# Performance work log

Measured on AMD Instinct MI355X. Metric: run time of the kernel, lower is better.

Reference implementation:

```python
import jax, jax.numpy as jnp
import numpy as np

N_NODES = 100000
N_EDGES = 3200000
N_FEAT = 512
N_HID = 16
N_CLS = 7


def setup_inputs() -> dict:
    key = jax.random.key(0)
    k0, k1, k2, k3 = jax.random.split(key, 4)
    x = jax.random.normal(k0, (N_NODES, N_FEAT), dtype=jnp.float32)
    edge_index = jax.random.randint(k1, (2, N_EDGES), 0, N_NODES, dtype=jnp.int64)
    W1 = jax.random.normal(k2, (N_FEAT, N_HID), dtype=jnp.float32) * (1.0 / np.sqrt(N_FEAT))
    b1 = jnp.zeros((N_HID,), dtype=jnp.float32)
    W2 = jax.random.normal(k3, (N_HID, N_CLS), dtype=jnp.float32) * (1.0 / np.sqrt(N_HID))
    b2 = jnp.zeros((N_CLS,), dtype=jnp.float32)
    return {"x": x, "edge_index": edge_index, "W1": W1, "b1": b1, "W2": W2, "b2": b2}


def _graph_conv(x, src, dst, W, b, n_nodes):
    # transform-then-aggregate: keeps the gathered edge tensor at hidden width
    h = x @ W                                      # [N, out]
    agg = jax.ops.segment_sum(h[src], dst, num_segments=n_nodes)  # [N, out]
    return agg + b


def reference(x, edge_index, W1, b1, W2, b2):
    src, dst = edge_index[0], edge_index[1]
    h = jax.nn.relu(_graph_conv(x, src, dst, W1, b1, N_NODES))
    # dropout is identity in eval mode
    out = _graph_conv(h, src, dst, W2, b2, N_NODES)
    return jax.nn.log_softmax(out, axis=1)
```

## Files before the change

kernel.cpp:

```cpp
#include <hip/hip_runtime.h>

#define NN 100000
#define NE 3200000
#define NF 512
#define NH 16
#define NC 7

__global__ __launch_bounds__(256) void gemm1_kernel(const float* __restrict__ x,
                                                    const float* __restrict__ W1,
                                                    float* __restrict__ h0) {
  const int lane = threadIdx.x & 63;
  const int wave = (blockIdx.x * blockDim.x + threadIdx.x) >> 6;
  const int nwaves = (gridDim.x * blockDim.x) >> 6;

  float w[8][NH];
#pragma unroll
  for (int i = 0; i < 4; ++i) {
#pragma unroll
    for (int j = 0; j < NH; ++j) {
      w[i][j]     = W1[(4 * lane + i) * NH + j];
      w[4 + i][j] = W1[(256 + 4 * lane + i) * NH + j];
    }
  }

  for (int row = wave; row < NN; row += nwaves) {
    const float4* xr = (const float4*)(x + (size_t)row * NF);
    float4 a0 = xr[lane];
    float4 a1 = xr[64 + lane];
    float a[8] = {a0.x, a0.y, a0.z, a0.w, a1.x, a1.y, a1.z, a1.w};

    float acc[NH];
#pragma unroll
    for (int j = 0; j < NH; ++j) acc[j] = 0.f;
#pragma unroll
    for (int i = 0; i < 8; ++i) {
#pragma unroll
      for (int j = 0; j < NH; ++j) acc[j] += a[i] * w[i][j];
    }

    float outv = 0.f;
#pragma unroll
    for (int j = 0; j < NH; ++j) {
      float v = acc[j];
      v += __shfl_xor(v, 1);
      v += __shfl_xor(v, 2);
      v += __shfl_xor(v, 4);
      v += __shfl_xor(v, 8);
      v += __shfl_xor(v, 16);
      v += __shfl_xor(v, 32);
      if (lane == j) outv = v;
    }
    if (lane < NH) h0[(size_t)row * NH + lane] = outv;
  }
}

__global__ __launch_bounds__(256) void scatter16_kernel(const int* __restrict__ ei,
                                                        const float* __restrict__ h0,
                                                        float* __restrict__ agg) {
  long long gid = (long long)blockIdx.x * blockDim.x + threadIdx.x;
  int e = (int)(gid >> 4);
  if (e >= NE) return;
  int j = (int)(gid & 15);
  int s = ei[e];
  int d = ei[NE + e];
  atomicAdd(&agg[(size_t)d * NH + j], h0[(size_t)s * NH + j]);
}

__global__ __launch_bounds__(256) void transform_kernel(const float* __restrict__ agg1,
                                                        const float* __restrict__ b1,
                                                        const float* __restrict__ W2,
                                                        float* __restrict__ p) {
  int n = blockIdx.x * blockDim.x + threadIdx.x;
  if (n >= NN) return;
  const float4* r = (const float4*)(agg1 + (size_t)n * NH);
  float4 v0 = r[0], v1 = r[1], v2 = r[2], v3 = r[3];
  float h[NH] = {v0.x, v0.y, v0.z, v0.w, v1.x, v1.y, v1.z, v1.w,
                 v2.x, v2.y, v2.z, v2.w, v3.x, v3.y, v3.z, v3.w};
#pragma unroll
  for (int k = 0; k < NH; ++k) h[k] = fmaxf(h[k] + b1[k], 0.f);

#pragma unroll
  for (int j = 0; j < NC; ++j) {
    float acc = 0.f;
#pragma unroll
    for (int k = 0; k < NH; ++k) acc += h[k] * W2[k * NC + j];
    p[(size_t)n * 8 + j] = acc;
  }
}

__global__ __launch_bounds__(256) void scatter7_kernel(const int* __restrict__ ei,
                                                       const float* __restrict__ p,
                                                       float* __restrict__ agg) {
  long long gid = (long long)blockIdx.x * blockDim.x + threadIdx.x;
  int e = (int)(gid >> 3);
  if (e >= NE) return;
  int j = (int)(gid & 7);
  if (j >= NC) return;
  int s = ei[e];
  int d = ei[NE + e];
  atomicAdd(&agg[(size_t)d * 8 + j], p[(size_t)s * 8 + j]);
}

__global__ __launch_bounds__(256) void lsm_kernel(const float* __restrict__ agg2,
                                                  const float* __restrict__ b2,
                                                  float* __restrict__ out) {
  int n = blockIdx.x * blockDim.x + threadIdx.x;
  if (n >= NN) return;
  float z[NC];
  float m = -1e30f;
#pragma unroll
  for (int j = 0; j < NC; ++j) {
    z[j] = agg2[(size_t)n * 8 + j] + b2[j];
    m = fmaxf(m, z[j]);
  }
  float s = 0.f;
#pragma unroll
  for (int j = 0; j < NC; ++j) s += __expf(z[j] - m);
  float l = __logf(s);
#pragma unroll
  for (int j = 0; j < NC; ++j) out[(size_t)n * NC + j] = z[j] - m - l;
}

extern "C" void kernel_launch(void* const* d_in, const int* in_sizes, int n_in,
                              void* d_out, int out_size, void* d_ws, size_t ws_size,
                              hipStream_t stream) {
  const float* x  = (const float*)d_in[0];
  const int*   ei = (const int*)d_in[1];
  const float* W1 = (const float*)d_in[2];
  const float* b1 = (const float*)d_in[3];
  const float* W2 = (const float*)d_in[4];
  const float* b2 = (const float*)d_in[5];
  float* out = (float*)d_out;

  float* bufA = (float*)d_ws;
  float* bufB = bufA + (size_t)NN * NH;

  hipMemsetAsync(bufB, 0, (size_t)NN * NH * sizeof(float), stream);
  gemm1_kernel<<<2048, 256, 0, stream>>>(x, W1, bufA);
  scatter16_kernel<<<(int)(((long long)NE * 16 + 255) / 256), 256, 0, stream>>>(ei, bufA, bufB);
  transform_kernel<<<(NN + 255) / 256, 256, 0, stream>>>(bufB, b1, W2, bufA);
  hipMemsetAsync(bufB, 0, (size_t)NN * 8 * sizeof(float), stream);
  scatter7_kernel<<<(int)(((long long)NE * 8 + 255) / 256), 256, 0, stream>>>(ei, bufA, bufB);
  lsm_kernel<<<(NN + 255) / 256, 256, 0, stream>>>(bufB, b2, out);
}
```

Measured before the change: 704.9 us.

## Build CSR by destination each call and replace atomic scatters with pull aggregation

Each call now builds a destination-sorted CSR (degree histogram, multi-level scan, permutation of sources). Both graph aggregations become atomic-free per-node gather reductions, and the second aggregation is fused with log-softmax. The first GEMM processes two rows per wave with a transpose-style shuffle reduction that needs fewer shuffles. This removes 80M float atomics at the cost of two edge passes with integer atomics and several small extra launches.

```diff
diff --git a/kernel.cpp b/kernel.cpp
--- a/kernel.cpp
+++ b/kernel.cpp
@@ -5,65 +5,172 @@
 #define NF 512
 #define NH 16
 #define NC 7
+#define NB ((NN + 255) / 256)
+
+__device__ __forceinline__ float reduce16(const float acc[16], int lane) {
+  float w8[8];
+#pragma unroll
+  for (int i = 0; i < 8; ++i) {
+    float sel = (lane & 1) ? acc[2 * i + 1] : acc[2 * i];
+    float oth = (lane & 1) ? acc[2 * i]     : acc[2 * i + 1];
+    w8[i] = sel + __shfl_xor(oth, 1);
+  }
+  float w4[4];
+#pragma unroll
+  for (int i = 0; i < 4; ++i) {
+    float sel = (lane & 2) ? w8[2 * i + 1] : w8[2 * i];
+    float oth = (lane & 2) ? w8[2 * i]     : w8[2 * i + 1];
+    w4[i] = sel + __shfl_xor(oth, 2);
+  }
+  float w2[2];
+#pragma unroll
+  for (int i = 0; i < 2; ++i) {
+    float sel = (lane & 4) ? w4[2 * i + 1] : w4[2 * i];
+    float oth = (lane & 4) ? w4[2 * i]     : w4[2 * i + 1];
+    w2[i] = sel + __shfl_xor(oth, 4);
+  }
+  float sel = (lane & 8) ? w2[1] : w2[0];
+  float oth = (lane & 8) ? w2[0] : w2[1];
+  float v = sel + __shfl_xor(oth, 8);
+  v += __shfl_xor(v, 16);
+  v += __shfl_xor(v, 32);
+  return v;
+}
 
 __global__ __launch_bounds__(256) void gemm1_kernel(const float* __restrict__ x,
                                                     const float* __restrict__ W1,
                                                     float* __restrict__ h0) {
   const int lane = threadIdx.x & 63;
   const int wave = (blockIdx.x * blockDim.x + threadIdx.x) >> 6;
-  const int nwaves = (gridDim.x * blockDim.x) >> 6;
+  const int nw   = (gridDim.x * blockDim.x) >> 6;
 
   float w[8][NH];
 #pragma unroll
-  for (int i = 0; i < 4; ++i) {
+  for (int i = 0; i < 4; ++i)
 #pragma unroll
     for (int j = 0; j < NH; ++j) {
       w[i][j]     = W1[(4 * lane + i) * NH + j];
       w[4 + i][j] = W1[(256 + 4 * lane + i) * NH + j];
     }
-  }
-
-  for (int row = wave; row < NN; row += nwaves) {
-    const float4* xr = (const float4*)(x + (size_t)row * NF);
-    float4 a0 = xr[lane];
-    float4 a1 = xr[64 + lane];
-    float a[8] = {a0.x, a0.y, a0.z, a0.w, a1.x, a1.y, a1.z, a1.w};
-
-    float acc[NH];
-#pragma unroll
-    for (int j = 0; j < NH; ++j) acc[j] = 0.f;
-#pragma unroll
-    for (int i = 0; i < 8; ++i) {
-#pragma unroll
-      for (int j = 0; j < NH; ++j) acc[j] += a[i] * w[i][j];
-    }
-
-    float outv = 0.f;
-#pragma unroll
-    for (int j = 0; j < NH; ++j) {
-      float v = acc[j];
-      v += __shfl_xor(v, 1);
-      v += __shfl_xor(v, 2);
-      v += __shfl_xor(v, 4);
-      v += __shfl_xor(v, 8);
-      v += __shfl_xor(v, 16);
-      v += __shfl_xor(v, 32);
-      if (lane == j) outv = v;
-    }
-    if (lane < NH) h0[(size_t)row * NH + lane] = outv;
-  }
-}
-
-__global__ __launch_bounds__(256) void scatter16_kernel(const int* __restrict__ ei,
-                                                        const float* __restrict__ h0,
-                                                        float* __restrict__ agg) {
-  long long gid = (long long)blockIdx.x * blockDim.x + threadIdx.x;
-  int e = (int)(gid >> 4);
+
+  for (int pr = wave; pr < NN / 2; pr += nw) {
+    int r0 = 2 * pr;
+    const float4* x0 = (const float4*)(x + (size_t)r0 * NF);
+    const float4* x1 = (const float4*)(x + (size_t)(r0 + 1) * NF);
+    float4 a0 = x0[lane], b0 = x0[64 + lane];
+    float4 a1 = x1[lane], b1 = x1[64 + lane];
+    float A0[8] = {a0.x, a0.y, a0.z, a0.w, b0.x, b0.y, b0.z, b0.w};
+    float A1[8] = {a1.x, a1.y, a1.z, a1.w, b1.x, b1.y, b1.z, b1.w};
+    float c0[NH], c1[NH];
+#pragma unroll
+    for (int j = 0; j < NH; ++j) { c0[j] = 0.f; c1[j] = 0.f; }
+#pragma unroll
+    for (int i = 0; i < 8; ++i)
+#pragma unroll
+      for (int j = 0; j < NH; ++j) {
+        c0[j] += A0[i] * w[i][j];
+        c1[j] += A1[i] * w[i][j];
+      }
+    float v0 = reduce16(c0, lane);
+    float v1 = reduce16(c1, lane);
+    if (lane < 16)      h0[(size_t)r0 * NH + lane] = v0;
+    else if (lane < 32) h0[(size_t)(r0 + 1) * NH + (lane & 15)] = v1;
+  }
+}
+
+__global__ __launch_bounds__(256) void hist_kernel(const int* __restrict__ ei,
+                                                   int* __restrict__ degcur) {
+  int e = blockIdx.x * blockDim.x + threadIdx.x;
+  if (e < NE) atomicAdd(&degcur[ei[NE + e]], 1);
+}
+
+__global__ __launch_bounds__(256) void bsum_kernel(const int* __restrict__ deg,
+                                                   int* __restrict__ bsum) {
+  int i = blockIdx.x * blockDim.x + threadIdx.x;
+  int lane = threadIdx.x & 63, wid = threadIdx.x >> 6;
+  int v = (i < NN) ? deg[i] : 0;
+#pragma unroll
+  for (int m = 1; m < 64; m <<= 1) v += __shfl_xor(v, m);
+  __shared__ int ws[4];
+  if (lane == 0) ws[wid] = v;
+  __syncthreads();
+  if (threadIdx.x == 0) bsum[blockIdx.x] = ws[0] + ws[1] + ws[2] + ws[3];
+}
+
+__global__ __launch_bounds__(512) void bscan_kernel(const int* __restrict__ bsum,
+                                                    int* __restrict__ boff) {
+  __shared__ int tmp[512];
+  int tid = threadIdx.x;
+  int v = (tid < NB) ? bsum[tid] : 0;
+  tmp[tid] = v;
+  __syncthreads();
+  for (int off = 1; off < 512; off <<= 1) {
+    int t = (tid >= off) ? tmp[tid - off] : 0;
+    __syncthreads();
+    tmp[tid] += t;
+    __syncthreads();
+  }
+  boff[tid] = tmp[tid] - v;
+}
+
+__global__ __launch_bounds__(256) void scan_final_kernel(int* __restrict__ degcur,
+                                                         const int* __restrict__ boff,
+                                                         int* __restrict__ rowstart) {
+  int i = blockIdx.x * blockDim.x + threadIdx.x;
+  int lane = threadIdx.x & 63, wid = threadIdx.x >> 6;
+  int v = (i < NN) ? degcur[i] : 0;
+  int sv = v;
+#pragma unroll
+  for (int d = 1; d < 64; d <<= 1) {
+    int t = __shfl_up(sv, d);
+    if (lane >= d) sv += t;
+  }
+  __shared__ int wsum[4];
+  if (lane == 63) wsum[wid] = sv;
+  __syncthreads();
+  int woff = 0;
+  for (int w = 0; w < wid; ++w) woff += wsum[w];
+  int excl = sv - v + woff + boff[blockIdx.x];
+  if (i < NN) {
+    rowstart[i] = excl;
+    degcur[i]   = excl;
+    if (i == NN - 1) rowstart[NN] = excl + v;
+  }
+}
+
+__global__ __launch_bounds__(256) void permute_kernel(const int* __restrict__ ei,
+                                                      int* __restrict__ cursor,
+                                                      int* __restrict__ ssrc) {
+  int e = blockIdx.x * blockDim.x + threadIdx.x;
   if (e >= NE) return;
-  int j = (int)(gid & 15);
-  int s = ei[e];
-  int d = ei[NE + e];
-  atomicAdd(&agg[(size_t)d * NH + j], h0[(size_t)s * NH + j]);
+  int s = ei[e], d = ei[NE + e];
+  int pos = atomicAdd(&cursor[d], 1);
+  ssrc[pos] = s;
+}
+
+__global__ __launch_bounds__(256) void agg1_kernel(const int* __restrict__ rowstart,
+                                                   const int* __restrict__ ssrc,
+                                                   const float* __restrict__ h0,
+                                                   float* __restrict__ agg1) {
+  int n = (blockIdx.x * blockDim.x + threadIdx.x) >> 6;
+  if (n >= NN) return;
+  int lane = threadIdx.x & 63;
+  int eg = lane >> 2, c = lane & 3;
+  int start = rowstart[n], end = rowstart[n + 1];
+  float4 acc = {0.f, 0.f, 0.f, 0.f};
+  for (int e = start + eg; e < end; e += 16) {
+    int s = ssrc[e];
+    float4 hv = *(const float4*)(h0 + (size_t)s * NH + 4 * c);
+    acc.x += hv.x; acc.y += hv.y; acc.z += hv.z; acc.w += hv.w;
+  }
+#pragma unroll
+  for (int m = 4; m < 64; m <<= 1) {
+    acc.x += __shfl_xor(acc.x, m);
+    acc.y += __shfl_xor(acc.y, m);
+    acc.z += __shfl_xor(acc.z, m);
+    acc.w += __shfl_xor(acc.w, m);
+  }
+  if (lane < 4) *(float4*)(agg1 + (size_t)n * NH + 4 * lane) = acc;
 }
 
 __global__ __launch_bounds__(256) void transform_kernel(const float* __restrict__ agg1,
@@ -78,7 +185,6 @@
                  v2.x, v2.y, v2.z, v2.w, v3.x, v3.y, v3.z, v3.w};
 #pragma unroll
   for (int k = 0; k < NH; ++k) h[k] = fmaxf(h[k] + b1[k], 0.f);
-
 #pragma unroll
   for (int j = 0; j < NC; ++j) {
     float acc = 0.f;
@@ -86,39 +192,35 @@
     for (int k = 0; k < NH; ++k) acc += h[k] * W2[k * NC + j];
     p[(size_t)n * 8 + j] = acc;
   }
-}
-
-__global__ __launch_bounds__(256) void scatter7_kernel(const int* __restrict__ ei,
+  p[(size_t)n * 8 + 7] = 0.f;
+}
+
+__global__ __launch_bounds__(256) void agg2_lsm_kernel(const int* __restrict__ rowstart,
+                                                       const int* __restrict__ ssrc,
                                                        const float* __restrict__ p,
-                                                       float* __restrict__ agg) {
-  long long gid = (long long)blockIdx.x * blockDim.x + threadIdx.x;
-  int e = (int)(gid >> 3);
-  if (e >= NE) return;
-  int j = (int)(gid & 7);
-  if (j >= NC) return;
-  int s = ei[e];
-  int d = ei[NE + e];
-  atomicAdd(&agg[(size_t)d * 8 + j], p[(size_t)s * 8 + j]);
-}
-
-__global__ __launch_bounds__(256) void lsm_kernel(const float* __restrict__ agg2,
-                                                  const float* __restrict__ b2,
-                                                  float* __restrict__ out) {
-  int n = blockIdx.x * blockDim.x + threadIdx.x;
+                                                       const float* __restrict__ b2,
+                                                       float* __restrict__ out) {
+  int n = (blockIdx.x * blockDim.x + threadIdx.x) >> 6;
   if (n >= NN) return;
-  float z[NC];
-  float m = -1e30f;
-#pragma unroll
-  for (int j = 0; j < NC; ++j) {
-    z[j] = agg2[(size_t)n * 8 + j] + b2[j];
-    m = fmaxf(m, z[j]);
-  }
-  float s = 0.f;
-#pragma unroll
-  for (int j = 0; j < NC; ++j) s += __expf(z[j] - m);
-  float l = __logf(s);
-#pragma unroll
-  for (int j = 0; j < NC; ++j) out[(size_t)n * NC + j] = z[j] - m - l;
+  int lane = threadIdx.x & 63;
+  int eg = lane >> 3, j = lane & 7;
+  int start = rowstart[n], end = rowstart[n + 1];
+  float acc = 0.f;
+  for (int e = start + eg; e < end; e += 8) {
+    int s = ssrc[e];
+    acc += p[(size_t)s * 8 + j];
+  }
+#pragma unroll
+  for (int m = 8; m < 64; m <<= 1) acc += __shfl_xor(acc, m);
+  float z = (j < NC) ? acc + b2[j] : -1e30f;
+  float mx = z;
+#pragma unroll
+  for (int m = 1; m < 8; m <<= 1) mx = fmaxf(mx, __shfl_xor(mx, m));
+  float ex = __expf(z - mx);
+  float s = ex;
+#pragma unroll
+  for (int m = 1; m < 8; m <<= 1) s += __shfl_xor(s, m);
+  if (j < NC) out[(size_t)n * NC + j] = z - mx - __logf(s);
 }
 
 extern "C" void kernel_launch(void* const* d_in, const int* in_sizes, int n_in,
@@ -132,14 +234,26 @@
   const float* b2 = (const float*)d_in[5];
   float* out = (float*)d_out;
 
-  float* bufA = (float*)d_ws;
-  float* bufB = bufA + (size_t)NN * NH;
-
-  hipMemsetAsync(bufB, 0, (size_t)NN * NH * sizeof(float), stream);
-  gemm1_kernel<<<2048, 256, 0, stream>>>(x, W1, bufA);
-  scatter16_kernel<<<(int)(((long long)NE * 16 + 255) / 256), 256, 0, stream>>>(ei, bufA, bufB);
-  transform_kernel<<<(NN + 255) / 256, 256, 0, stream>>>(bufB, b1, W2, bufA);
-  hipMemsetAsync(bufB, 0, (size_t)NN * 8 * sizeof(float), stream);
-  scatter7_kernel<<<(int)(((long long)NE * 8 + 255) / 256), 256, 0, stream>>>(ei, bufA, bufB);
-  lsm_kernel<<<(NN + 255) / 256, 256, 0, stream>>>(bufB, b2, out);
-}
+  float* h0      = (float*)d_ws;
+  float* agg1    = h0 + (size_t)NN * NH;
+  int*   rowstart= (int*)(agg1 + (size_t)NN * NH);
+  int*   degcur  = rowstart + NN + 1;
+  int*   bsum    = degcur + NN;
+  int*   boff    = bsum + 512;
+  int*   ssrc    = boff + 512;
+  float* p       = h0;
+
+  const int EB = (NE + 255) / 256;
+
+  hipMemsetAsync(degcur, 0, (size_t)NN * sizeof(int), stream);
+  hist_kernel<<<EB, 256, 0, stream>>>(ei, degcur);
+  bsum_kernel<<<NB, 256, 0, stream>>>(degcur, bsum);
+  bscan_kernel<<<1, 512, 0, stream>>>(bsum, boff);
+  scan_final_kernel<<<NB, 256, 0, stream>>>(degcur, boff, rowstart);
+  permute_kernel<<<EB, 256, 0, stream>>>(ei, degcur, ssrc);
+
+  gemm1_kernel<<<2048, 256, 0, stream>>>(x, W1, h0);
+  agg1_kernel<<<(NN * 64 + 255) / 256, 256, 0, stream>>>(rowstart, ssrc, h0, agg1);
+  transform_kernel<<<(NN + 255) / 256, 256, 0, stream>>>(agg1, b1, W2, p);
+  agg2_lsm_kernel<<<(NN * 64 + 255) / 256, 256, 0, stream>>>(rowstart, ssrc, p, b2, out);
+}
```

Result: slower. 803.7 us (+14.0%).
